# Kernel tuning notes

Measured on AMD Instinct MI355X. Metric: run time of the kernel, lower is better.

The kernel has to match this reference:

```python
import jax, jax.numpy as jnp
import numpy as np

N = 50000          # nodes
E = 800000         # edges
D_IN = 64          # env INPUT_DIM
D_H = 64           # env HIDDEN_DIM
D_OUT = 32         # env OUTPUT_DIM
A_H = 16           # action HIDDEN_DIM
NUM_ENV = 3        # env NUM_LAYERS
TAU = 1.0          # gumbel temperature (fixed, LEARN_TEMPERATURE=False)
LN_EPS = 1e-5


def setup_inputs() -> dict:
    key = jax.random.key(0)
    ks = jax.random.split(key, 24)

    def lin(k, fan_in, fan_out):
        s = 1.0 / np.sqrt(fan_in)
        kw, kb = jax.random.split(k)
        W = jax.random.uniform(kw, (fan_in, fan_out), jnp.float32, -s, s)
        b = jax.random.uniform(kb, (fan_out,), jnp.float32, -s, s)
        return W, b

    inp = {}
    inp['x'] = jax.random.normal(ks[0], (N, D_IN), jnp.float32)
    inp['edge_index'] = jax.random.randint(ks[1], (2, E), 0, N, dtype=jnp.int32)

    inp['W_enc'], inp['b_enc'] = lin(ks[2], D_IN, D_H)
    env_W, env_b = [], []
    for l in range(NUM_ENV):
        W, b = lin(ks[3 + l], 2 * D_H, D_H)
        env_W.append(W); env_b.append(b)
    inp['env_W'] = jnp.stack(env_W)   # [NUM_ENV, 2*D_H, D_H]
    inp['env_b'] = jnp.stack(env_b)   # [NUM_ENV, D_H]
    inp['W_dec'], inp['b_dec'] = lin(ks[6], D_H, D_OUT)
    inp['ln_g'] = jnp.ones((D_H,), jnp.float32)
    inp['ln_b'] = jnp.zeros((D_H,), jnp.float32)
    inp['in_W1'], inp['in_b1'] = lin(ks[7], 2 * D_H, A_H)
    inp['in_W2'], inp['in_b2'] = lin(ks[8], 2 * A_H, 2)
    inp['out_W1'], inp['out_b1'] = lin(ks[9], 2 * D_H, A_H)
    inp['out_W2'], inp['out_b2'] = lin(ks[10], 2 * A_H, 2)
    return inp


def _layernorm(x, g, b):
    mu = jnp.mean(x, axis=-1, keepdims=True)
    var = jnp.var(x, axis=-1, keepdims=True)
    return (x - mu) * jax.lax.rsqrt(var + LN_EPS) * g + b


def _conv(x, src, dst, W, b, edge_weight=None):
    # WeightedGNNConv: gather x[src] -> (optional * edge_weight) -> scatter-add at dst -> lin(concat(x, agg))
    msg = x[src]                                   # [E, d]
    if edge_weight is not None:
        msg = msg * edge_weight[:, None]
    agg = jax.ops.segment_sum(msg, dst, num_segments=N)
    return jnp.concatenate([x, agg], axis=-1) @ W + b


def _action_net(x, src, dst, W1, b1, W2, b2):
    h = jax.nn.relu(_conv(x, src, dst, W1, b1))
    return _conv(h, src, dst, W2, b2)              # [N, 2] logits


def _gumbel_hard(logits, key, tau):
    u = jax.random.uniform(key, logits.shape, logits.dtype, 1e-20, 1.0)
    g = -jnp.log(-jnp.log(u))
    y = jax.nn.softmax((logits + g) / tau, axis=-1)
    y_hard = jax.nn.one_hot(jnp.argmax(y, axis=-1), logits.shape[-1], dtype=y.dtype)
    return y + jax.lax.stop_gradient(y_hard - y)   # straight-through


def reference(x, edge_index, W_enc, b_enc, env_W, env_b, W_dec, b_dec, ln_g, ln_b,
              in_W1, in_b1, in_W2, in_b2, out_W1, out_b1, out_W2, out_b2):
    src, dst = edge_index[0], edge_index[1]        # u, v
    h = x @ W_enc + b_enc                          # encoder (dropout is identity in eval)
    noise_key = jax.random.key(1234)
    ews = []
    for l in range(NUM_ENV):
        h = _layernorm(h, ln_g, ln_b)
        in_logits = _action_net(h, src, dst, in_W1, in_b1, in_W2, in_b2)
        out_logits = _action_net(h, src, dst, out_W1, out_b1, out_W2, out_b2)
        in_p = _gumbel_hard(in_logits, jax.random.fold_in(noise_key, 2 * l), TAU)
        out_p = _gumbel_hard(out_logits, jax.random.fold_in(noise_key, 2 * l + 1), TAU)
        # create_edge_weight: keep_in_prob[v] * keep_out_prob[u]
        ew = in_p[:, 0][dst] * out_p[:, 0][src]    # [E], values in {0,1}
        ews.append(ew)
        h = _conv(h, src, dst, env_W[l], env_b[l], edge_weight=ew)
    out = h @ W_dec + b_dec
    return out, jnp.stack(ews)
```

## Files before the change

### kernel.cpp

```cpp
#include <hip/hip_runtime.h>
#include <math.h>

static constexpr int NN = 50000;
static constexpr int EE = 800000;

#define SHFL_ADD4(v, off) { v.x += __shfl_xor(v.x, off, 64); v.y += __shfl_xor(v.y, off, 64); \
                            v.z += __shfl_xor(v.z, off, 64); v.w += __shfl_xor(v.w, off, 64); }

struct TF2 { unsigned a, b; };

__host__ __device__ __forceinline__ TF2 tf2x32(unsigned k0, unsigned k1,
                                               unsigned x0, unsigned x1) {
  unsigned k2 = k0 ^ k1 ^ 0x1BD11BDAu;
  x0 += k0; x1 += k1;
#define TFR(r) { x0 += x1; x1 = (x1 << (r)) | (x1 >> (32 - (r))); x1 ^= x0; }
  TFR(13) TFR(15) TFR(26) TFR(6)
  x0 += k1; x1 += k2 + 1u;
  TFR(17) TFR(29) TFR(16) TFR(24)
  x0 += k2; x1 += k0 + 2u;
  TFR(13) TFR(15) TFR(26) TFR(6)
  x0 += k0; x1 += k1 + 3u;
  TFR(17) TFR(29) TFR(16) TFR(24)
  x0 += k1; x1 += k2 + 4u;
  TFR(13) TFR(15) TFR(26) TFR(6)
  x0 += k2; x1 += k0 + 5u;
#undef TFR
  TF2 r; r.a = x0; r.b = x1; return r;
}

__device__ __forceinline__ float u01_bits(unsigned w) {
  float fl = __uint_as_float((w >> 9) | 0x3f800000u) - 1.0f;
  return fmaxf(1e-20f, fl + 1e-20f);
}

__device__ __forceinline__ float keep01(float l0, float l1, unsigned k0, unsigned k1, int node) {
  unsigned f0 = 2u * (unsigned)node, f1 = f0 + 1u;
  TF2 t0 = tf2x32(k0, k1, 0u, f0);
  TF2 t1 = tf2x32(k0, k1, 0u, f1);
  float g0 = -logf(-logf(u01_bits(t0.a ^ t0.b)));
  float g1 = -logf(-logf(u01_bits(t1.a ^ t1.b)));
  float z0 = l0 + g0, z1 = l1 + g1;
  float m  = fmaxf(z0, z1);
  float e0 = expf(z0 - m), e1 = expf(z1 - m);
  float s  = e0 + e1;
  float y0 = e0 / s, y1 = e1 / s;
  return (y1 > y0) ? 0.0f : 1.0f;
}

__global__ void k_count(const int* __restrict__ dst, int* __restrict__ deg, int e) {
  int i = blockIdx.x * blockDim.x + threadIdx.x;
  if (i < e) atomicAdd(&deg[dst[i]], 1);
}

__global__ void k_bsum(const int* __restrict__ deg, int* __restrict__ bsum, int n) {
  int i = blockIdx.x * 256 + threadIdx.x;
  int v = (i < n) ? deg[i] : 0;
  #pragma unroll
  for (int off = 32; off; off >>= 1) v += __shfl_xor(v, off, 64);
  __shared__ int ws[4];
  if ((threadIdx.x & 63) == 0) ws[threadIdx.x >> 6] = v;
  __syncthreads();
  if (threadIdx.x == 0) bsum[blockIdx.x] = ws[0] + ws[1] + ws[2] + ws[3];
}

__global__ void k_bscan(const int* __restrict__ bsum, int* __restrict__ bpref,
                        int nb, int* __restrict__ row_ptr, int n) {
  __shared__ int s[256];
  int t = threadIdx.x;
  int v = (t < nb) ? bsum[t] : 0;
  s[t] = v; __syncthreads();
  for (int off = 1; off < 256; off <<= 1) {
    int u = (t >= off) ? s[t - off] : 0;
    __syncthreads();
    s[t] += u;
    __syncthreads();
  }
  bpref[t] = s[t] - v;
  if (t == 0) row_ptr[n] = s[255];
}

__global__ void k_prefix(const int* __restrict__ deg, const int* __restrict__ bpref,
                         int* __restrict__ row_ptr, int* __restrict__ cursor, int n) {
  __shared__ int s[256];
  int t = threadIdx.x;
  int i = blockIdx.x * 256 + t;
  int v = (i < n) ? deg[i] : 0;
  s[t] = v; __syncthreads();
  for (int off = 1; off < 256; off <<= 1) {
    int u = (t >= off) ? s[t - off] : 0;
    __syncthreads();
    s[t] += u;
    __syncthreads();
  }
  if (i < n) {
    int ex = s[t] - v + bpref[blockIdx.x];
    row_ptr[i] = ex; cursor[i] = ex;
  }
}

__global__ void k_fill(const int* __restrict__ src, const int* __restrict__ dst,
                       int* __restrict__ cursor, int* __restrict__ col, int e) {
  int i = blockIdx.x * blockDim.x + threadIdx.x;
  if (i < e) {
    int pos = atomicAdd(&cursor[dst[i]], 1);
    col[pos] = src[i];
  }
}

__global__ void k_enc_ln(const float* __restrict__ x, const float* __restrict__ W,
                         const float* __restrict__ bias, const float* __restrict__ g,
                         const float* __restrict__ bb, float* __restrict__ hln) {
  __shared__ float Ws[64 * 64];
  for (int i = threadIdx.x; i < 64 * 64; i += 256) Ws[i] = W[i];
  __syncthreads();
  int node = blockIdx.x * 4 + (threadIdx.x >> 6);
  int j = threadIdx.x & 63;
  const float* xr = x + (size_t)node * 64;
  float s = bias[j];
  #pragma unroll
  for (int i = 0; i < 64; i++) s = fmaf(xr[i], Ws[i * 64 + j], s);
  float t = s;
  #pragma unroll
  for (int off = 32; off; off >>= 1) t += __shfl_xor(t, off, 64);
  float mu = t * (1.0f / 64.0f);
  float d = s - mu;
  float q = d * d;
  #pragma unroll
  for (int off = 32; off; off >>= 1) q += __shfl_xor(q, off, 64);
  float rs = 1.0f / sqrtf(q * (1.0f / 64.0f) + 1e-5f);
  hln[(size_t)node * 64 + j] = d * rs * g[j] + bb[j];
}

__global__ void k_projAll(const float* __restrict__ hln, const float* __restrict__ envW,
                          const float* __restrict__ envb,
                          const float* __restrict__ W1i, const float* __restrict__ W1o,
                          float* __restrict__ Htop, float* __restrict__ Pbot,
                          float* __restrict__ P1, float* __restrict__ S1, int nchunk) {
  __shared__ float Ws[128 * 64];
  __shared__ float st[256];
  int t = threadIdx.x;
  for (int i = t; i < 128 * 64; i += 256) Ws[i] = envW[i];
  int w = t >> 6, lane = t & 63;
  int h = lane >> 5, jo = lane & 31;
  const float* Wg = (jo < 16) ? W1i : W1o;
  int colw = jo & 15;
  float wr[64];
  #pragma unroll
  for (int i = 0; i < 64; i++) wr[i] = Wg[(h * 64 + i) * 16 + colw];
  float bj = envb[lane];
  for (int blk = blockIdx.x; blk < nchunk; blk += gridDim.x) {
    __syncthreads();
    st[t] = hln[(size_t)blk * 256 + t];
    __syncthreads();
    const float* sv = &st[w * 64];
    float a = bj, b = 0.f, c = 0.f;
    #pragma unroll
    for (int i = 0; i < 64; i++) {
      float hv = sv[i];
      a = fmaf(hv, Ws[i * 64 + lane], a);
      b = fmaf(hv, Ws[(64 + i) * 64 + lane], b);
      c = fmaf(hv, wr[i], c);
    }
    size_t node = (size_t)blk * 4 + w;
    Htop[node * 64 + lane] = a;
    Pbot[node * 64 + lane] = b;
    if (h == 0) S1[node * 32 + jo] = c;
    else        P1[node * 32 + jo] = c;
  }
}

__global__ void k_gatherA(const float* __restrict__ P1, const float* __restrict__ S1,
                          const int* __restrict__ row_ptr, const int* __restrict__ col,
                          const float* __restrict__ inb1, const float* __restrict__ outb1,
                          const float* __restrict__ inW2, const float* __restrict__ outW2,
                          float* __restrict__ P2S2) {
  int t = threadIdx.x;
  int w = t >> 6, lane = t & 63;
  int es = lane >> 3, f4 = lane & 7;
  int node = blockIdx.x * 4 + w;
  int b = row_ptr[node], e = row_ptr[node + 1];
  float4 acc = make_float4(0.f, 0.f, 0.f, 0.f);
  for (int base = b; base < e; base += 16) {
    int i0 = base + es, i1 = base + 8 + es;
    if (i0 < e) {
      float4 v = ((const float4*)(P1 + (size_t)col[i0] * 32))[f4];
      acc.x += v.x; acc.y += v.y; acc.z += v.z; acc.w += v.w;
    }
    if (i1 < e) {
      float4 v = ((const float4*)(P1 + (size_t)col[i1] * 32))[f4];
      acc.x += v.x; acc.y += v.y; acc.z += v.z; acc.w += v.w;
    }
  }
  SHFL_ADD4(acc, 8) SHFL_ADD4(acc, 16) SHFL_ADD4(acc, 32)
  float4 s1 = ((const float4*)(S1 + (size_t)node * 32))[f4];
  const float* bsrc = (f4 < 4) ? inb1 : outb1;
  const float* W2   = (f4 < 4) ? inW2 : outW2;
  int jb = (f4 & 3) * 4;
  float4 b4 = *(const float4*)(bsrc + jb);
  float r0 = fmaxf(s1.x + acc.x + b4.x, 0.f);
  float r1 = fmaxf(s1.y + acc.y + b4.y, 0.f);
  float r2 = fmaxf(s1.z + acc.z + b4.z, 0.f);
  float r3 = fmaxf(s1.w + acc.w + b4.w, 0.f);
  float pa0, pa1, pb0, pb1;
  {
    const float* Wc = W2 + jb * 2;
    pa0 = r0 * Wc[0] + r1 * Wc[2] + r2 * Wc[4] + r3 * Wc[6];
    pa1 = r0 * Wc[1] + r1 * Wc[3] + r2 * Wc[5] + r3 * Wc[7];
    const float* Wd = W2 + (16 + jb) * 2;
    pb0 = r0 * Wd[0] + r1 * Wd[2] + r2 * Wd[4] + r3 * Wd[6];
    pb1 = r0 * Wd[1] + r1 * Wd[3] + r2 * Wd[5] + r3 * Wd[7];
  }
  pa0 += __shfl_xor(pa0, 1, 64); pa0 += __shfl_xor(pa0, 2, 64);
  pa1 += __shfl_xor(pa1, 1, 64); pa1 += __shfl_xor(pa1, 2, 64);
  pb0 += __shfl_xor(pb0, 1, 64); pb0 += __shfl_xor(pb0, 2, 64);
  pb1 += __shfl_xor(pb1, 1, 64); pb1 += __shfl_xor(pb1, 2, 64);
  float* row = P2S2 + (size_t)node * 8;
  if (lane == 0) { row[0] = pb0; row[1] = pb1; row[4] = pa0; row[5] = pa1; }
  if (lane == 4) { row[2] = pb0; row[3] = pb1; row[6] = pa0; row[7] = pa1; }
}

__global__ void k_gatherB(const float* __restrict__ P2S2, const int* __restrict__ row_ptr,
                          const int* __restrict__ col,
                          const float* __restrict__ inb2, const float* __restrict__ outb2,
                          float* __restrict__ keep_in, float* __restrict__ keep_out,
                          unsigned ki0, unsigned ki1, unsigned ko0, unsigned ko1) {
  int t = threadIdx.x;
  int w = t >> 6, lane = t & 63;
  int g = lane >> 4, el = lane & 15;
  int node = blockIdx.x * 16 + w * 4 + g;
  int b = row_ptr[node], e = row_ptr[node + 1];
  float a0 = 0.f, a1 = 0.f, a2 = 0.f, a3 = 0.f;
  for (int base = b; base < e; base += 16) {
    int idx = base + el;
    if (idx < e) {
      int u = col[idx];
      float4 p = *(const float4*)(P2S2 + (size_t)u * 8);
      a0 += p.x; a1 += p.y; a2 += p.z; a3 += p.w;
    }
  }
  #pragma unroll
  for (int off = 8; off; off >>= 1) {
    a0 += __shfl_xor(a0, off, 64);
    a1 += __shfl_xor(a1, off, 64);
    a2 += __shfl_xor(a2, off, 64);
    a3 += __shfl_xor(a3, off, 64);
  }
  float4 sf = *(const float4*)(P2S2 + (size_t)node * 8 + 4);
  if (el == 0)
    keep_in[node]  = keep01(sf.x + a0 + inb2[0],  sf.y + a1 + inb2[1],  ki0, ki1, node);
  else if (el == 1)
    keep_out[node] = keep01(sf.z + a2 + outb2[0], sf.w + a3 + outb2[1], ko0, ko1, node);
}

template <bool LN>
__global__ void k_aggD(const float* __restrict__ Htop, const float* __restrict__ Pbot,
                       const int* __restrict__ row_ptr, const int* __restrict__ col,
                       const int* __restrict__ src, const int* __restrict__ dst,
                       const float* __restrict__ keep_in, const float* __restrict__ keep_out,
                       float* __restrict__ ew, const float* __restrict__ g,
                       const float* __restrict__ bb, float* __restrict__ hout) {
  int t = threadIdx.x;
  int ei = blockIdx.x * 64 + t;
  if (t < 64 && ei < EE)
    ew[ei] = keep_in[dst[ei]] * keep_out[src[ei]];

  int w = t >> 6, lane = t & 63;
  int es = lane >> 4, f4 = lane & 15;
  int node = blockIdx.x * 4 + w;
  float ki = keep_in[node];
  int b = row_ptr[node], e = row_ptr[node + 1];
  float4 acc = make_float4(0.f, 0.f, 0.f, 0.f);
  if (ki != 0.f) {
    for (int base = b; base < e; base += 8) {
      int i0 = base + es, i1 = base + 4 + es;
      int u0 = 0, u1 = 0; float ko0 = 0.f, ko1 = 0.f;
      if (i0 < e) { u0 = col[i0]; ko0 = keep_out[u0]; }
      if (i1 < e) { u1 = col[i1]; ko1 = keep_out[u1]; }
      if (ko0 != 0.f) {
        float4 v = ((const float4*)(Pbot + (size_t)u0 * 64))[f4];
        acc.x += v.x; acc.y += v.y; acc.z += v.z; acc.w += v.w;
      }
      if (ko1 != 0.f) {
        float4 v = ((const float4*)(Pbot + (size_t)u1 * 64))[f4];
        acc.x += v.x; acc.y += v.y; acc.z += v.z; acc.w += v.w;
      }
    }
  }
  SHFL_ADD4(acc, 16) SHFL_ADD4(acc, 32)
  float4 hv = ((const float4*)(Htop + (size_t)node * 64))[f4];
  float4 a;
  a.x = fmaf(acc.x, ki, hv.x);
  a.y = fmaf(acc.y, ki, hv.y);
  a.z = fmaf(acc.z, ki, hv.z);
  a.w = fmaf(acc.w, ki, hv.w);
  if (LN) {
    float ps = (a.x + a.y) + (a.z + a.w);
    ps += __shfl_xor(ps, 1, 64); ps += __shfl_xor(ps, 2, 64);
    ps += __shfl_xor(ps, 4, 64); ps += __shfl_xor(ps, 8, 64);
    float mu = ps * (1.0f / 64.0f);
    float4 d; d.x = a.x - mu; d.y = a.y - mu; d.z = a.z - mu; d.w = a.w - mu;
    float q = (d.x * d.x + d.y * d.y) + (d.z * d.z + d.w * d.w);
    q += __shfl_xor(q, 1, 64); q += __shfl_xor(q, 2, 64);
    q += __shfl_xor(q, 4, 64); q += __shfl_xor(q, 8, 64);
    float rs = 1.0f / sqrtf(q * (1.0f / 64.0f) + 1e-5f);
    if (es == 0) {
      float4 g4 = ((const float4*)g)[f4];
      float4 b4 = ((const float4*)bb)[f4];
      float4 o;
      o.x = d.x * rs * g4.x + b4.x;
      o.y = d.y * rs * g4.y + b4.y;
      o.z = d.z * rs * g4.z + b4.z;
      o.w = d.w * rs * g4.w + b4.w;
      ((float4*)(hout + (size_t)node * 64))[f4] = o;
    }
  } else {
    if (es == 0)
      ((float4*)(hout + (size_t)node * 64))[f4] = a;
  }
}

__global__ void k_dec(const float* __restrict__ h, const float* __restrict__ W,
                      const float* __restrict__ bias, float* __restrict__ out) {
  __shared__ float Ws[64 * 32];
  int t = threadIdx.x;
  for (int i = t; i < 64 * 32; i += 256) Ws[i] = W[i];
  __syncthreads();
  int node = blockIdx.x * 8 + (t >> 5);
  int j = t & 31;
  const float* hr = h + (size_t)node * 64;
  float s = bias[j];
  #pragma unroll
  for (int i = 0; i < 64; i++) s = fmaf(hr[i], Ws[i * 32 + j], s);
  out[(size_t)node * 32 + j] = s;
}

extern "C" void kernel_launch(void* const* d_in, const int* in_sizes, int n_in,
                              void* d_out, int out_size, void* d_ws, size_t ws_size,
                              hipStream_t stream) {
  const float* x      = (const float*)d_in[0];
  const int*   ei     = (const int*)  d_in[1];
  const float* W_enc  = (const float*)d_in[2];
  const float* b_enc  = (const float*)d_in[3];
  const float* env_W  = (const float*)d_in[4];
  const float* env_b  = (const float*)d_in[5];
  const float* W_dec  = (const float*)d_in[6];
  const float* b_dec  = (const float*)d_in[7];
  const float* ln_g   = (const float*)d_in[8];
  const float* ln_b   = (const float*)d_in[9];
  const float* in_W1  = (const float*)d_in[10];
  const float* in_b1  = (const float*)d_in[11];
  const float* in_W2  = (const float*)d_in[12];
  const float* in_b2  = (const float*)d_in[13];
  const float* out_W1 = (const float*)d_in[14];
  const float* out_b1 = (const float*)d_in[15];
  const float* out_W2 = (const float*)d_in[16];
  const float* out_b2 = (const float*)d_in[17];

  const int n = NN, e = EE;
  const int* src = ei;
  const int* dst = ei + e;

  float* out_h  = (float*)d_out;
  float* out_ew = out_h + (size_t)n * 32;

  size_t off = 0;
  auto alloc = [&](size_t bytes) -> void* {
    void* p = (char*)d_ws + off;
    off += (bytes + 255) & ~(size_t)255;
    return p;
  };
  float* hlnA    = (float*)alloc((size_t)n * 64 * 4);
  float* hlnB    = (float*)alloc((size_t)n * 64 * 4);
  float* Htop    = (float*)alloc((size_t)n * 64 * 4);
  float* Pbot    = (float*)alloc((size_t)n * 64 * 4);
  float* P1      = (float*)alloc((size_t)n * 32 * 4);
  float* S1      = (float*)alloc((size_t)n * 32 * 4);
  float* P2S2    = (float*)alloc((size_t)n * 8 * 4);
  float* keep_i  = (float*)alloc((size_t)n * 4);
  float* keep_o  = (float*)alloc((size_t)n * 4);
  int*   deg     = (int*)alloc((size_t)n * 4);
  int*   row_ptr = (int*)alloc((size_t)(n + 1) * 4);
  int*   cursor  = (int*)alloc((size_t)n * 4);
  int*   bsum    = (int*)alloc(256 * 4);
  int*   bpref   = (int*)alloc(256 * 4);
  int*   colA    = (int*)alloc((size_t)e * 4);
  if (off > ws_size) return;

  const int nb = (n + 255) / 256;

  hipMemsetAsync(deg, 0, (size_t)n * 4, stream);
  k_count<<<(e + 255) / 256, 256, 0, stream>>>(dst, deg, e);
  k_bsum<<<nb, 256, 0, stream>>>(deg, bsum, n);
  k_bscan<<<1, 256, 0, stream>>>(bsum, bpref, nb, row_ptr, n);
  k_prefix<<<nb, 256, 0, stream>>>(deg, bpref, row_ptr, cursor, n);
  k_fill<<<(e + 255) / 256, 256, 0, stream>>>(src, dst, cursor, colA, e);

  const int g4  = n / 4;
  const int g8  = n / 8;
  const int g16 = n / 16;

  k_enc_ln<<<g4, 256, 0, stream>>>(x, W_enc, b_enc, ln_g, ln_b, hlnA);

  float* hln = hlnA;
  float* hln_next = hlnB;
  for (int l = 0; l < 3; l++) {
    TF2 kin  = tf2x32(0u, 1234u, 0u, (unsigned)(2 * l));
    TF2 kout = tf2x32(0u, 1234u, 0u, (unsigned)(2 * l + 1));

    k_projAll<<<1250, 256, 0, stream>>>(hln, env_W + (size_t)l * 128 * 64,
                                        env_b + (size_t)l * 64, in_W1, out_W1,
                                        Htop, Pbot, P1, S1, g4);
    k_gatherA<<<g4, 256, 0, stream>>>(P1, S1, row_ptr, colA, in_b1, out_b1,
                                      in_W2, out_W2, P2S2);
    k_gatherB<<<g16, 256, 0, stream>>>(P2S2, row_ptr, colA, in_b2, out_b2,
                                       keep_i, keep_o, kin.a, kin.b, kout.a, kout.b);
    if (l < 2) {
      k_aggD<true><<<g4, 256, 0, stream>>>(Htop, Pbot, row_ptr, colA, src, dst,
                                           keep_i, keep_o, out_ew + (size_t)l * e,
                                           ln_g, ln_b, hln_next);
    } else {
      k_aggD<false><<<g4, 256, 0, stream>>>(Htop, Pbot, row_ptr, colA, src, dst,
                                            keep_i, keep_o, out_ew + (size_t)l * e,
                                            ln_g, ln_b, hln_next);
    }
    float* tmp = hln; hln = hln_next; hln_next = tmp;
  }

  k_dec<<<g8, 256, 0, stream>>>(hln, W_dec, b_dec, out_h);
}
```

Baseline: 659.3 us.

## Remap dense projections to one thread per node with register accumulators

The encoder+LayerNorm, the per-layer projection and the decoder kernels now give each thread a whole node row instead of one output column. Each thread accumulates all outputs in registers and reads weights with wave-uniform global loads, replacing the shared-memory weight staging and cross-lane LayerNorm shuffles. The goal is to cut LDS traffic and synchronisation in these small matmuls and to write outputs as vector stores. The cost is very high register use, up to 192 accumulators in the projection kernel, which risks spills and low occupancy, plus strided per-thread row loads.

```diff
diff --git a/kernel.cpp b/kernel.cpp
--- a/kernel.cpp
+++ b/kernel.cpp
@@ -107,66 +107,129 @@
   }
 }
 
-__global__ void k_enc_ln(const float* __restrict__ x, const float* __restrict__ W,
-                         const float* __restrict__ bias, const float* __restrict__ g,
-                         const float* __restrict__ bb, float* __restrict__ hln) {
-  __shared__ float Ws[64 * 64];
-  for (int i = threadIdx.x; i < 64 * 64; i += 256) Ws[i] = W[i];
-  __syncthreads();
-  int node = blockIdx.x * 4 + (threadIdx.x >> 6);
-  int j = threadIdx.x & 63;
+__global__ __launch_bounds__(64) void k_encB(const float* __restrict__ x,
+                        const float* __restrict__ W, const float* __restrict__ bias,
+                        const float* __restrict__ g, const float* __restrict__ bb,
+                        float* __restrict__ hln, int n) {
+  int node = blockIdx.x * 64 + threadIdx.x;
+  bool act = node < n;
   const float* xr = x + (size_t)node * 64;
-  float s = bias[j];
-  #pragma unroll
-  for (int i = 0; i < 64; i++) s = fmaf(xr[i], Ws[i * 64 + j], s);
-  float t = s;
-  #pragma unroll
-  for (int off = 32; off; off >>= 1) t += __shfl_xor(t, off, 64);
-  float mu = t * (1.0f / 64.0f);
-  float d = s - mu;
-  float q = d * d;
-  #pragma unroll
-  for (int off = 32; off; off >>= 1) q += __shfl_xor(q, off, 64);
+  float a[64];
+  #pragma unroll
+  for (int j = 0; j < 64; j++) a[j] = bias[j];
+  for (int i = 0; i < 64; i += 4) {
+    float4 hv = act ? *(const float4*)(xr + i) : make_float4(0.f, 0.f, 0.f, 0.f);
+    #pragma unroll
+    for (int j = 0; j < 64; j++) {
+      a[j] = fmaf(hv.x, W[(i    ) * 64 + j], a[j]);
+      a[j] = fmaf(hv.y, W[(i + 1) * 64 + j], a[j]);
+      a[j] = fmaf(hv.z, W[(i + 2) * 64 + j], a[j]);
+      a[j] = fmaf(hv.w, W[(i + 3) * 64 + j], a[j]);
+    }
+  }
+  if (!act) return;
+  float s = 0.f;
+  #pragma unroll
+  for (int j = 0; j < 64; j++) s += a[j];
+  float mu = s * (1.0f / 64.0f);
+  float q = 0.f;
+  #pragma unroll
+  for (int j = 0; j < 64; j++) { float d = a[j] - mu; q += d * d; }
   float rs = 1.0f / sqrtf(q * (1.0f / 64.0f) + 1e-5f);
-  hln[(size_t)node * 64 + j] = d * rs * g[j] + bb[j];
-}
-
-__global__ void k_projAll(const float* __restrict__ hln, const float* __restrict__ envW,
-                          const float* __restrict__ envb,
-                          const float* __restrict__ W1i, const float* __restrict__ W1o,
-                          float* __restrict__ Htop, float* __restrict__ Pbot,
-                          float* __restrict__ P1, float* __restrict__ S1, int nchunk) {
-  __shared__ float Ws[128 * 64];
-  __shared__ float st[256];
-  int t = threadIdx.x;
-  for (int i = t; i < 128 * 64; i += 256) Ws[i] = envW[i];
-  int w = t >> 6, lane = t & 63;
-  int h = lane >> 5, jo = lane & 31;
-  const float* Wg = (jo < 16) ? W1i : W1o;
-  int colw = jo & 15;
-  float wr[64];
-  #pragma unroll
-  for (int i = 0; i < 64; i++) wr[i] = Wg[(h * 64 + i) * 16 + colw];
-  float bj = envb[lane];
-  for (int blk = blockIdx.x; blk < nchunk; blk += gridDim.x) {
-    __syncthreads();
-    st[t] = hln[(size_t)blk * 256 + t];
-    __syncthreads();
-    const float* sv = &st[w * 64];
-    float a = bj, b = 0.f, c = 0.f;
+  float* out = hln + (size_t)node * 64;
+  #pragma unroll
+  for (int qd = 0; qd < 16; qd++) {
+    float4 o;
+    o.x = (a[4*qd  ] - mu) * rs * g[4*qd  ] + bb[4*qd  ];
+    o.y = (a[4*qd+1] - mu) * rs * g[4*qd+1] + bb[4*qd+1];
+    o.z = (a[4*qd+2] - mu) * rs * g[4*qd+2] + bb[4*qd+2];
+    o.w = (a[4*qd+3] - mu) * rs * g[4*qd+3] + bb[4*qd+3];
+    ((float4*)out)[qd] = o;
+  }
+}
+
+__global__ __launch_bounds__(64) void k_projB(const float* __restrict__ hln,
+                        const float* __restrict__ envW, const float* __restrict__ envb,
+                        const float* __restrict__ W1i, const float* __restrict__ W1o,
+                        float* __restrict__ Htop, float* __restrict__ Pbot,
+                        float* __restrict__ P1, float* __restrict__ S1, int n) {
+  int node = blockIdx.x * 64 + threadIdx.x;
+  bool act = node < n;
+  const float* hr = hln + (size_t)node * 64;
+  float aH[64], aP[64], aS[32], aQ[32];
+  #pragma unroll
+  for (int j = 0; j < 64; j++) { aH[j] = envb[j]; aP[j] = 0.f; }
+  #pragma unroll
+  for (int j = 0; j < 32; j++) { aS[j] = 0.f; aQ[j] = 0.f; }
+
+#define PROJ_STEP(hv, i) {                                                   \
+    const float* w0 = envW + (i) * 64;                                       \
+    const float* w1 = envW + (64 + (i)) * 64;                                \
+    _Pragma("unroll")                                                        \
+    for (int j = 0; j < 64; j++) {                                           \
+      aH[j] = fmaf(hv, w0[j], aH[j]);                                        \
+      aP[j] = fmaf(hv, w1[j], aP[j]);                                        \
+    }                                                                        \
+    const float* u0 = W1i + (i) * 16;  const float* u1 = W1i + (64 + (i)) * 16; \
+    const float* v0 = W1o + (i) * 16;  const float* v1 = W1o + (64 + (i)) * 16; \
+    _Pragma("unroll")                                                        \
+    for (int j = 0; j < 16; j++) {                                           \
+      aS[j]      = fmaf(hv, u0[j], aS[j]);                                   \
+      aS[16 + j] = fmaf(hv, v0[j], aS[16 + j]);                              \
+      aQ[j]      = fmaf(hv, u1[j], aQ[j]);                                   \
+      aQ[16 + j] = fmaf(hv, v1[j], aQ[16 + j]);                              \
+    }                                                                        \
+  }
+
+  for (int i = 0; i < 64; i += 4) {
+    float4 hv = act ? *(const float4*)(hr + i) : make_float4(0.f, 0.f, 0.f, 0.f);
+    PROJ_STEP(hv.x, i)
+    PROJ_STEP(hv.y, i + 1)
+    PROJ_STEP(hv.z, i + 2)
+    PROJ_STEP(hv.w, i + 3)
+  }
+#undef PROJ_STEP
+  if (!act) return;
+  float* oh = Htop + (size_t)node * 64;
+  float* op = Pbot + (size_t)node * 64;
+  #pragma unroll
+  for (int q = 0; q < 16; q++) {
+    ((float4*)oh)[q] = make_float4(aH[4*q], aH[4*q+1], aH[4*q+2], aH[4*q+3]);
+    ((float4*)op)[q] = make_float4(aP[4*q], aP[4*q+1], aP[4*q+2], aP[4*q+3]);
+  }
+  float* os = S1 + (size_t)node * 32;
+  float* oq = P1 + (size_t)node * 32;
+  #pragma unroll
+  for (int q = 0; q < 8; q++) {
+    ((float4*)os)[q] = make_float4(aS[4*q], aS[4*q+1], aS[4*q+2], aS[4*q+3]);
+    ((float4*)oq)[q] = make_float4(aQ[4*q], aQ[4*q+1], aQ[4*q+2], aQ[4*q+3]);
+  }
+}
+
+__global__ __launch_bounds__(64) void k_decB(const float* __restrict__ h,
+                        const float* __restrict__ W, const float* __restrict__ bias,
+                        float* __restrict__ out, int n) {
+  int node = blockIdx.x * 64 + threadIdx.x;
+  bool act = node < n;
+  const float* hr = h + (size_t)node * 64;
+  float a[32];
+  #pragma unroll
+  for (int j = 0; j < 32; j++) a[j] = bias[j];
+  for (int i = 0; i < 64; i += 4) {
+    float4 hv = act ? *(const float4*)(hr + i) : make_float4(0.f, 0.f, 0.f, 0.f);
     #pragma unroll
-    for (int i = 0; i < 64; i++) {
-      float hv = sv[i];
-      a = fmaf(hv, Ws[i * 64 + lane], a);
-      b = fmaf(hv, Ws[(64 + i) * 64 + lane], b);
-      c = fmaf(hv, wr[i], c);
-    }
-    size_t node = (size_t)blk * 4 + w;
-    Htop[node * 64 + lane] = a;
-    Pbot[node * 64 + lane] = b;
-    if (h == 0) S1[node * 32 + jo] = c;
-    else        P1[node * 32 + jo] = c;
-  }
+    for (int j = 0; j < 32; j++) {
+      a[j] = fmaf(hv.x, W[(i    ) * 32 + j], a[j]);
+      a[j] = fmaf(hv.y, W[(i + 1) * 32 + j], a[j]);
+      a[j] = fmaf(hv.z, W[(i + 2) * 32 + j], a[j]);
+      a[j] = fmaf(hv.w, W[(i + 3) * 32 + j], a[j]);
+    }
+  }
+  if (!act) return;
+  float* o = out + (size_t)node * 32;
+  #pragma unroll
+  for (int q = 0; q < 8; q++)
+    ((float4*)o)[q] = make_float4(a[4*q], a[4*q+1], a[4*q+2], a[4*q+3]);
 }
 
 __global__ void k_gatherA(const float* __restrict__ P1, const float* __restrict__ S1,
@@ -319,21 +382,6 @@
   }
 }
 
-__global__ void k_dec(const float* __restrict__ h, const float* __restrict__ W,
-                      const float* __restrict__ bias, float* __restrict__ out) {
-  __shared__ float Ws[64 * 32];
-  int t = threadIdx.x;
-  for (int i = t; i < 64 * 32; i += 256) Ws[i] = W[i];
-  __syncthreads();
-  int node = blockIdx.x * 8 + (t >> 5);
-  int j = t & 31;
-  const float* hr = h + (size_t)node * 64;
-  float s = bias[j];
-  #pragma unroll
-  for (int i = 0; i < 64; i++) s = fmaf(hr[i], Ws[i * 32 + j], s);
-  out[(size_t)node * 32 + j] = s;
-}
-
 extern "C" void kernel_launch(void* const* d_in, const int* in_sizes, int n_in,
                               void* d_out, int out_size, void* d_ws, size_t ws_size,
                               hipStream_t stream) {
@@ -396,10 +444,10 @@
   k_fill<<<(e + 255) / 256, 256, 0, stream>>>(src, dst, cursor, colA, e);
 
   const int g4  = n / 4;
-  const int g8  = n / 8;
   const int g16 = n / 16;
-
-  k_enc_ln<<<g4, 256, 0, stream>>>(x, W_enc, b_enc, ln_g, ln_b, hlnA);
+  const int gw  = (n + 63) / 64;
+
+  k_encB<<<gw, 64, 0, stream>>>(x, W_enc, b_enc, ln_g, ln_b, hlnA, n);
 
   float* hln = hlnA;
   float* hln_next = hlnB;
@@ -407,9 +455,9 @@
     TF2 kin  = tf2x32(0u, 1234u, 0u, (unsigned)(2 * l));
     TF2 kout = tf2x32(0u, 1234u, 0u, (unsigned)(2 * l + 1));
 
-    k_projAll<<<1250, 256, 0, stream>>>(hln, env_W + (size_t)l * 128 * 64,
-                                        env_b + (size_t)l * 64, in_W1, out_W1,
-                                        Htop, Pbot, P1, S1, g4);
+    k_projB<<<gw, 64, 0, stream>>>(hln, env_W + (size_t)l * 128 * 64,
+                                   env_b + (size_t)l * 64, in_W1, out_W1,
+                                   Htop, Pbot, P1, S1, n);
     k_gatherA<<<g4, 256, 0, stream>>>(P1, S1, row_ptr, colA, in_b1, out_b1,
                                       in_W2, out_W2, P2S2);
     k_gatherB<<<g16, 256, 0, stream>>>(P2S2, row_ptr, colA, in_b2, out_b2,
@@ -426,5 +474,5 @@
     float* tmp = hln; hln = hln_next; hln_next = tmp;
   }
 
-  k_dec<<<g8, 256, 0, stream>>>(hln, W_dec, b_dec, out_h);
-}
+  k_decB<<<gw, 64, 0, stream>>>(hln, W_dec, b_dec, out_h, n);
+}
```

Result: slower. 804.1 us (+22.0%).

## Rewrite dense projections as register-weight wavefronts with readlane broadcast

Applied to the files above, without the earlier changes.

Replaces the shared-memory-based encoder, projection and decoder kernels with wavefront kernels that keep a weight column per lane in registers. Each wave walks 64 nodes in turn, loading one node row at a time (prefetching the next) and broadcasting its elements with readlane instead of reading LDS. The projection kernel now splits its outputs across three waves per block. The aim is to cut LDS traffic and syncs. In exchange it needs many more registers and has less node-level parallelism per block, since 64 nodes are handled one after another.

```diff
diff --git a/kernel.cpp b/kernel.cpp
--- a/kernel.cpp
+++ b/kernel.cpp
@@ -6,6 +6,10 @@
 
 #define SHFL_ADD4(v, off) { v.x += __shfl_xor(v.x, off, 64); v.y += __shfl_xor(v.y, off, 64); \
                             v.z += __shfl_xor(v.z, off, 64); v.w += __shfl_xor(v.w, off, 64); }
+
+__device__ __forceinline__ float bcast(float v, int i) {
+  return __uint_as_float(__builtin_amdgcn_readlane(__float_as_uint(v), i));
+}
 
 struct TF2 { unsigned a, b; };
 
@@ -107,65 +111,111 @@
   }
 }
 
-__global__ void k_enc_ln(const float* __restrict__ x, const float* __restrict__ W,
-                         const float* __restrict__ bias, const float* __restrict__ g,
-                         const float* __restrict__ bb, float* __restrict__ hln) {
-  __shared__ float Ws[64 * 64];
-  for (int i = threadIdx.x; i < 64 * 64; i += 256) Ws[i] = W[i];
-  __syncthreads();
-  int node = blockIdx.x * 4 + (threadIdx.x >> 6);
-  int j = threadIdx.x & 63;
-  const float* xr = x + (size_t)node * 64;
-  float s = bias[j];
-  #pragma unroll
-  for (int i = 0; i < 64; i++) s = fmaf(xr[i], Ws[i * 64 + j], s);
-  float t = s;
-  #pragma unroll
-  for (int off = 32; off; off >>= 1) t += __shfl_xor(t, off, 64);
-  float mu = t * (1.0f / 64.0f);
-  float d = s - mu;
-  float q = d * d;
-  #pragma unroll
-  for (int off = 32; off; off >>= 1) q += __shfl_xor(q, off, 64);
-  float rs = 1.0f / sqrtf(q * (1.0f / 64.0f) + 1e-5f);
-  hln[(size_t)node * 64 + j] = d * rs * g[j] + bb[j];
-}
-
-__global__ void k_projAll(const float* __restrict__ hln, const float* __restrict__ envW,
-                          const float* __restrict__ envb,
-                          const float* __restrict__ W1i, const float* __restrict__ W1o,
-                          float* __restrict__ Htop, float* __restrict__ Pbot,
-                          float* __restrict__ P1, float* __restrict__ S1, int nchunk) {
-  __shared__ float Ws[128 * 64];
-  __shared__ float st[256];
-  int t = threadIdx.x;
-  for (int i = t; i < 128 * 64; i += 256) Ws[i] = envW[i];
-  int w = t >> 6, lane = t & 63;
-  int h = lane >> 5, jo = lane & 31;
-  const float* Wg = (jo < 16) ? W1i : W1o;
-  int colw = jo & 15;
+__global__ __launch_bounds__(64) void k_encC(const float* __restrict__ x,
+                        const float* __restrict__ W, const float* __restrict__ bias,
+                        const float* __restrict__ g, const float* __restrict__ bb,
+                        float* __restrict__ hln, int n) {
+  int lane = threadIdx.x;
   float wr[64];
   #pragma unroll
-  for (int i = 0; i < 64; i++) wr[i] = Wg[(h * 64 + i) * 16 + colw];
-  float bj = envb[lane];
-  for (int blk = blockIdx.x; blk < nchunk; blk += gridDim.x) {
-    __syncthreads();
-    st[t] = hln[(size_t)blk * 256 + t];
-    __syncthreads();
-    const float* sv = &st[w * 64];
-    float a = bj, b = 0.f, c = 0.f;
-    #pragma unroll
-    for (int i = 0; i < 64; i++) {
-      float hv = sv[i];
-      a = fmaf(hv, Ws[i * 64 + lane], a);
-      b = fmaf(hv, Ws[(64 + i) * 64 + lane], b);
-      c = fmaf(hv, wr[i], c);
-    }
-    size_t node = (size_t)blk * 4 + w;
-    Htop[node * 64 + lane] = a;
-    Pbot[node * 64 + lane] = b;
-    if (h == 0) S1[node * 32 + jo] = c;
-    else        P1[node * 32 + jo] = c;
+  for (int i = 0; i < 64; i++) wr[i] = W[i * 64 + lane];
+  float bs = bias[lane], gg = g[lane], bbv = bb[lane];
+  int base = blockIdx.x * 64;
+  int cnt = min(64, n - base);
+  float hv = x[(size_t)base * 64 + lane];
+  for (int nd = 0; nd < cnt; nd++) {
+    int node = base + nd;
+    float hvn = (nd + 1 < cnt) ? x[(size_t)(node + 1) * 64 + lane] : 0.f;
+    float a0 = bs, a1 = 0.f;
+    #pragma unroll
+    for (int i = 0; i < 64; i += 2) {
+      a0 = fmaf(bcast(hv, i),     wr[i],     a0);
+      a1 = fmaf(bcast(hv, i + 1), wr[i + 1], a1);
+    }
+    float acc = a0 + a1;
+    float t = acc;
+    #pragma unroll
+    for (int off = 32; off; off >>= 1) t += __shfl_xor(t, off, 64);
+    float mu = t * (1.0f / 64.0f);
+    float d = acc - mu;
+    float q = d * d;
+    #pragma unroll
+    for (int off = 32; off; off >>= 1) q += __shfl_xor(q, off, 64);
+    float rs = 1.0f / sqrtf(q * (1.0f / 64.0f) + 1e-5f);
+    hln[(size_t)node * 64 + lane] = d * rs * gg + bbv;
+    hv = hvn;
+  }
+}
+
+__global__ __launch_bounds__(192) void k_projD(const float* __restrict__ hln,
+                        const float* __restrict__ envW, const float* __restrict__ envb,
+                        const float* __restrict__ W1i, const float* __restrict__ W1o,
+                        float* __restrict__ Htop, float* __restrict__ Pbot,
+                        float* __restrict__ P1, float* __restrict__ S1, int n) {
+  int w = threadIdx.x >> 6, lane = threadIdx.x & 63;
+  float wr[64];
+  float bias0 = 0.f;
+  float* outp;
+  size_t ostride;
+  int ooff;
+  if (w == 0) {
+    #pragma unroll
+    for (int i = 0; i < 64; i++) wr[i] = envW[i * 64 + lane];
+    bias0 = envb[lane];
+    outp = Htop; ostride = 64; ooff = lane;
+  } else if (w == 1) {
+    #pragma unroll
+    for (int i = 0; i < 64; i++) wr[i] = envW[(64 + i) * 64 + lane];
+    outp = Pbot; ostride = 64; ooff = lane;
+  } else {
+    int grp = lane >> 4, c = lane & 15;
+    const float* Wb = (grp & 1) ? W1o : W1i;
+    int roff = (grp & 2) ? 64 : 0;
+    #pragma unroll
+    for (int i = 0; i < 64; i++) wr[i] = Wb[(roff + i) * 16 + c];
+    outp = (grp & 2) ? P1 : S1;
+    ostride = 32; ooff = ((grp & 1) ? 16 : 0) + c;
+  }
+  int base = blockIdx.x * 64;
+  int cnt = min(64, n - base);
+  float hv = hln[(size_t)base * 64 + lane];
+  for (int nd = 0; nd < cnt; nd++) {
+    int node = base + nd;
+    float hvn = (nd + 1 < cnt) ? hln[(size_t)(node + 1) * 64 + lane] : 0.f;
+    float a0 = bias0, a1 = 0.f;
+    #pragma unroll
+    for (int i = 0; i < 64; i += 2) {
+      a0 = fmaf(bcast(hv, i),     wr[i],     a0);
+      a1 = fmaf(bcast(hv, i + 1), wr[i + 1], a1);
+    }
+    outp[(size_t)node * ostride + ooff] = a0 + a1;
+    hv = hvn;
+  }
+}
+
+__global__ __launch_bounds__(64) void k_decC(const float* __restrict__ h,
+                        const float* __restrict__ W, const float* __restrict__ bias,
+                        float* __restrict__ out, int n) {
+  int lane = threadIdx.x;
+  int c = lane & 31;
+  float wr[64];
+  #pragma unroll
+  for (int i = 0; i < 64; i++) wr[i] = W[i * 32 + c];
+  float bs = bias[c];
+  int base = blockIdx.x * 64;
+  int cnt = min(64, n - base);
+  float hv = h[(size_t)base * 64 + lane];
+  for (int nd = 0; nd < cnt; nd++) {
+    int node = base + nd;
+    float hvn = (nd + 1 < cnt) ? h[(size_t)(node + 1) * 64 + lane] : 0.f;
+    float a0 = bs, a1 = 0.f;
+    #pragma unroll
+    for (int i = 0; i < 64; i += 2) {
+      a0 = fmaf(bcast(hv, i),     wr[i],     a0);
+      a1 = fmaf(bcast(hv, i + 1), wr[i + 1], a1);
+    }
+    if (lane < 32) out[(size_t)node * 32 + c] = a0 + a1;
+    hv = hvn;
   }
 }
 
@@ -319,21 +369,6 @@
   }
 }
 
-__global__ void k_dec(const float* __restrict__ h, const float* __restrict__ W,
-                      const float* __restrict__ bias, float* __restrict__ out) {
-  __shared__ float Ws[64 * 32];
-  int t = threadIdx.x;
-  for (int i = t; i < 64 * 32; i += 256) Ws[i] = W[i];
-  __syncthreads();
-  int node = blockIdx.x * 8 + (t >> 5);
-  int j = t & 31;
-  const float* hr = h + (size_t)node * 64;
-  float s = bias[j];
-  #pragma unroll
-  for (int i = 0; i < 64; i++) s = fmaf(hr[i], Ws[i * 32 + j], s);
-  out[(size_t)node * 32 + j] = s;
-}
-
 extern "C" void kernel_launch(void* const* d_in, const int* in_sizes, int n_in,
                               void* d_out, int out_size, void* d_ws, size_t ws_size,
                               hipStream_t stream) {
@@ -396,10 +431,10 @@
   k_fill<<<(e + 255) / 256, 256, 0, stream>>>(src, dst, cursor, colA, e);
 
   const int g4  = n / 4;
-  const int g8  = n / 8;
   const int g16 = n / 16;
-
-  k_enc_ln<<<g4, 256, 0, stream>>>(x, W_enc, b_enc, ln_g, ln_b, hlnA);
+  const int gw  = (n + 63) / 64;
+
+  k_encC<<<gw, 64, 0, stream>>>(x, W_enc, b_enc, ln_g, ln_b, hlnA, n);
 
   float* hln = hlnA;
   float* hln_next = hlnB;
@@ -407,9 +442,9 @@
     TF2 kin  = tf2x32(0u, 1234u, 0u, (unsigned)(2 * l));
     TF2 kout = tf2x32(0u, 1234u, 0u, (unsigned)(2 * l + 1));
 
-    k_projAll<<<1250, 256, 0, stream>>>(hln, env_W + (size_t)l * 128 * 64,
-                                        env_b + (size_t)l * 64, in_W1, out_W1,
-                                        Htop, Pbot, P1, S1, g4);
+    k_projD<<<gw, 192, 0, stream>>>(hln, env_W + (size_t)l * 128 * 64,
+                                    env_b + (size_t)l * 64, in_W1, out_W1,
+                                    Htop, Pbot, P1, S1, n);
     k_gatherA<<<g4, 256, 0, stream>>>(P1, S1, row_ptr, colA, in_b1, out_b1,
                                       in_W2, out_W2, P2S2);
     k_gatherB<<<g16, 256, 0, stream>>>(P2S2, row_ptr, colA, in_b2, out_b2,
@@ -426,5 +461,5 @@
     float* tmp = hln; hln = hln_next; hln_next = tmp;
   }
 
-  k_dec<<<g8, 256, 0, stream>>>(hln, W_dec, b_dec, out_h);
-}
+  k_decC<<<gw, 64, 0, stream>>>(hln, W_dec, b_dec, out_h, n);
+}
```

Result: slower. 695.2 us (+5.4%).
